# Kernel optimization log

Hardware: AMD Instinct MI355X
Metric: run time of the kernel (lower is better)

## Reference

```python
import jax, jax.numpy as jnp
import numpy as np

B, S, H, M = 8, 128, 768, 128
EPS = 1e-12


def setup_inputs() -> dict:
    key = jax.random.key(0)
    ks = jax.random.split(key, 8)
    seq_hiddens = jax.random.normal(ks[0], (B, S, H), dtype=jnp.float32)
    gamma = jnp.ones((H,), jnp.float32)
    beta = jnp.zeros((H,), jnp.float32)
    # conditional LN dense weights (torch Linear weight: (out, in)); small init so math stays stable
    w_beta = jax.random.normal(ks[1], (H, H), dtype=jnp.float32) * 0.02
    w_gamma = jax.random.normal(ks[2], (H, H), dtype=jnp.float32) * 0.02
    w_ent = jax.random.normal(ks[3], (H, M), dtype=jnp.float32) * 0.02
    w_head = jax.random.normal(ks[4], (H, M), dtype=jnp.float32) * 0.02
    w_tail = jax.random.normal(ks[5], (H, M), dtype=jnp.float32) * 0.02
    b_ent = jnp.zeros((M,), jnp.float32)
    b_head = jnp.zeros((M,), jnp.float32)
    b_tail = jnp.zeros((M,), jnp.float32)
    return dict(seq_hiddens=seq_hiddens, gamma=gamma, beta=beta, w_beta=w_beta,
                w_gamma=w_gamma, w_ent=w_ent, b_ent=b_ent, w_head=w_head,
                b_head=b_head, w_tail=w_tail, b_tail=b_tail)


def _handshake_cln(seq, gamma, beta, w_beta, w_gamma):
    # Triangular pair expansion in the same row-major order as the torch loop:
    # for ind in range(S): pairs (ind, ind), (ind, ind+1), ..., (ind, S-1)
    s = seq.shape[1]
    ii, jj = jnp.triu_indices(s)                 # (P,) each, P = S(S+1)/2
    x = seq[:, jj, :]                            # visible hiddens   (B, P, H)
    cond = seq[:, ii, :]                         # repeated hiddens  (B, P, H)
    beta_c = jnp.einsum('bph,oh->bpo', cond, w_beta) + beta      # (B, P, H)
    gamma_c = jnp.einsum('bph,oh->bpo', cond, w_gamma) + gamma   # (B, P, H)
    mean = jnp.mean(x, axis=-1, keepdims=True)
    out = x - mean
    var = jnp.mean(out * out, axis=-1, keepdims=True)
    std = (var + EPS) ** 2                       # NOTE: faithful to source (no sqrt)
    return out / std * gamma_c + beta_c


def reference(seq_hiddens, gamma, beta, w_beta, w_gamma, w_ent, b_ent,
              w_head, b_head, w_tail, b_tail):
    shaking = _handshake_cln(seq_hiddens, gamma, beta, w_beta, w_gamma)  # (B, P, H)
    ent = jnp.tanh(shaking @ w_ent + b_ent)      # (B, P, M)
    head = jnp.tanh(shaking @ w_head + b_head)
    tail = jnp.tanh(shaking @ w_tail + b_tail)
    return jnp.stack([ent, head, tail], axis=0)  # (3, B, P, M)
```

## Files before the change

### kernel.cpp

```cpp
#include <hip/hip_runtime.h>
#include <hip/hip_bf16.h>
#include <hip/hip_fp16.h>
#include <math.h>

#define B_   8
#define S_   128
#define H_   768
#define M_   128
#define P_   8256
#define BP_  66048
#define EPSF 1e-12f

typedef unsigned short u16;
typedef unsigned int   u32;
typedef _Float16 h16;
typedef _Float16 ffrag __attribute__((ext_vector_type(8)));
typedef float    f32x16 __attribute__((ext_vector_type(16)));

__device__ __forceinline__ u32 fuse2(u32 x, u32 g, u32 b) {
    __half2 r = __hfma2(__builtin_bit_cast(__half2, x),
                        __builtin_bit_cast(__half2, g),
                        __builtin_bit_cast(__half2, b));
    return __builtin_bit_cast(u32, r);
}
__device__ __forceinline__ float fast_tanh(float v) {
    float t = __expf(v + v);
    float r = __builtin_amdgcn_rcpf(t + 1.0f);
    return fmaf(-2.0f, r, 1.0f);
}
__device__ __forceinline__ void gl_lds16(const h16* g, h16* l) {
    __builtin_amdgcn_global_load_lds(
        (const __attribute__((address_space(1))) u32*)g,
        (__attribute__((address_space(3))) u32*)l, 16, 0, 0);
}

#define NORM0 5763
__global__ void k_prep(const float* __restrict__ seq,
                       const float* __restrict__ wg, const float* __restrict__ wb,
                       const float* __restrict__ we, const float* __restrict__ wh,
                       const float* __restrict__ wt,
                       const float* __restrict__ be, const float* __restrict__ bh,
                       const float* __restrict__ bt,
                       h16* __restrict__ wgb, h16* __restrict__ wbb,
                       h16* __restrict__ wpk, float* __restrict__ biasc,
                       h16* __restrict__ xn, h16* __restrict__ condb)
{
    __shared__ float red[4];
    const int bx = blockIdx.x;
    const int t = threadIdx.x;

    if (bx < NORM0) {
        int idx = bx * 256 + t;
        if (idx < 589824) {
            wgb[idx] = (h16)wg[idx];
        } else if (idx < 1179648) {
            int i = idx - 589824;
            wbb[i] = (h16)wb[i];
        } else if (idx < 1474560) {
            int i = idx - 1179648;
            int e  = i & 7;
            int n  = (i >> 3) & 127;
            int v  = i >> 10;
            int ch = v & 3;
            int w2 = v >> 2;
            int kt = w2 % 24;
            int nb = w2 / 24;
            int h  = kt * 32 + ch * 8 + e;
            const float* src = (nb == 0) ? we : (nb == 1 ? wh : wt);
            wpk[i] = (h16)src[h * 128 + n];
        } else if (idx < 1474944) {
            int n = idx - 1474560;
            biasc[n] = (n < 128) ? be[n] : (n < 256 ? bh[n - 128] : bt[n - 256]);
        }
        return;
    }
    const int row = bx - NORM0;
    const int lane = t & 63, wid = t >> 6;
    const float* x = seq + (size_t)row * H_;
    float x0 = x[t], x1 = x[t + 256], x2 = x[t + 512];

    float s = x0 + x1 + x2;
    for (int o = 32; o; o >>= 1) s += __shfl_xor(s, o);
    if (lane == 0) red[wid] = s;
    __syncthreads();
    float mean = (red[0] + red[1] + red[2] + red[3]) * (1.0f / 768.0f);

    float c0 = x0 - mean, c1 = x1 - mean, c2 = x2 - mean;
    float ss = c0 * c0 + c1 * c1 + c2 * c2;
    for (int o = 32; o; o >>= 1) ss += __shfl_xor(ss, o);
    __syncthreads();
    if (lane == 0) red[wid] = ss;
    __syncthreads();
    float var = (red[0] + red[1] + red[2] + red[3]) * (1.0f / 768.0f);
    float sd = var + EPSF;
    float scale = 1.0f / (sd * sd);

    h16* xr = xn + (size_t)row * H_;
    h16* cr = condb + (size_t)row * H_;
    xr[t] = (h16)(c0 * scale); xr[t + 256] = (h16)(c1 * scale); xr[t + 512] = (h16)(c2 * scale);
    cr[t] = (h16)x0;           cr[t + 256] = (h16)x1;           cr[t + 512] = (h16)x2;
}

__global__ __launch_bounds__(256) void k_cond_gemm(
    const h16* __restrict__ Ab, const h16* __restrict__ Wg, const h16* __restrict__ Wb,
    const float* __restrict__ gamma, const float* __restrict__ beta,
    h16* __restrict__ Gc, h16* __restrict__ Bc)
{
    __shared__ h16 Ash[64 * 72];
    __shared__ h16 Bsh[32 * 72];
    const int t = threadIdx.x;
    const int row0 = blockIdx.x * 64;
    const int by = blockIdx.y;
    const bool isg = (by < 24);
    const int nc0 = (isg ? by : by - 24) * 32;
    const h16* wsrc = isg ? Wg : Wb;

    const int r = t >> 2, q = t & 3;
    const h16* ap = Ab + (size_t)(row0 + r) * H_ + q * 16;
    h16* asto = &Ash[r * 72 + q * 16];
    const int rb = t >> 3, qb = t & 7;
    const h16* wp = wsrc + (size_t)(nc0 + rb) * H_ + qb * 8;
    h16* bsto = &Bsh[rb * 72 + qb * 8];

    const int lane = t & 63, wid = t >> 6;
    const int wm0 = (wid >> 1) * 32, wn0 = (wid & 1) * 16;
    const int l15 = lane & 15, quad = lane >> 4, q8 = quad * 8;

    typedef float f32x4 __attribute__((ext_vector_type(4)));
    f32x4 acc[2] = {};
    for (int kt = 0; kt < 12; ++kt) {
        const int k0 = kt * 64;
        uint4 a0 = *(const uint4*)(ap + k0); uint4 a1 = *(const uint4*)(ap + k0 + 8);
        uint4 w0 = *(const uint4*)(wp + k0);
        *(uint4*)asto = a0; *(uint4*)(asto + 8) = a1;
        *(uint4*)bsto = w0;
        __syncthreads();
#pragma unroll
        for (int ks = 0; ks < 64; ks += 32) {
            ffrag af[2], bf;
#pragma unroll
            for (int mi = 0; mi < 2; ++mi)
                af[mi] = *reinterpret_cast<const ffrag*>(&Ash[(wm0 + mi * 16 + l15) * 72 + ks + q8]);
            bf = *reinterpret_cast<const ffrag*>(&Bsh[(wn0 + l15) * 72 + ks + q8]);
#pragma unroll
            for (int mi = 0; mi < 2; ++mi)
                acc[mi] = __builtin_amdgcn_mfma_f32_16x16x32_f16(af[mi], bf, acc[mi], 0, 0, 0);
        }
        __syncthreads();
    }

    const float* bias = isg ? gamma : beta;
    h16* outp = isg ? Gc : Bc;
#pragma unroll
    for (int mi = 0; mi < 2; ++mi) {
        int c = wn0 + l15;
        float bv = bias[nc0 + c];
#pragma unroll
        for (int reg = 0; reg < 4; ++reg) {
            int rg = wm0 + mi * 16 + quad * 4 + reg;
            outp[(size_t)(row0 + rg) * H_ + nc0 + c] = (h16)(acc[mi][reg] + bv);
        }
    }
}

__global__ __launch_bounds__(256, 6) void k_pair_gemm(
    const h16* __restrict__ Xn, const h16* __restrict__ Gcb, const h16* __restrict__ Bcb,
    const h16* __restrict__ Wpk, const float* __restrict__ biasc,
    float* __restrict__ out)
{
    __shared__ h16 Ash[2][4 * 64 * 8];
    __shared__ h16 Bsh[2][4 * 128 * 8];

    const int t = threadIdx.x;
    const int nb = blockIdx.x;
    const int row0 = blockIdx.y * 64;

    const int r_s = t >> 2, c4 = t & 3;
    int gp = row0 + r_s;
    int b = gp / P_;
    int p = gp - b * P_;
    int i = (int)((257.0f - sqrtf(66049.0f - 8.0f * (float)p)) * 0.5f);
    if (i < 0) i = 0; if (i > 127) i = 127;
    while (i > 0 && (i * (257 - i)) / 2 > p) --i;
    while (((i + 1) * (256 - i)) / 2 <= p) ++i;
    int j = i + (p - (i * (257 - i)) / 2);

    const h16* xp  = Xn  + (size_t)(b * 128 + j) * H_ + c4 * 8;
    const h16* gp_ = Gcb + (size_t)(b * 128 + i) * H_ + c4 * 8;
    const h16* bp_ = Bcb + (size_t)(b * 128 + i) * H_ + c4 * 8;
    const int aw = (c4 * 64 + r_s) * 8;

    const h16* wtile = Wpk + (size_t)nb * 24 * 4096;
    const int wud = t & ~63;

    const int lane = t & 63, wid = t >> 6;
    const int wm0 = (wid >> 1) * 32, wn0 = (wid & 1) * 64;
    const int l31 = lane & 31, hi = lane >> 5;

#pragma unroll
    for (int c = 0; c < 2; ++c)
        gl_lds16(wtile + (size_t)(c * 256 + t) * 8, &Bsh[0][(c * 256 + wud) * 8]);
    {
        uint4 xa = *(const uint4*)xp;
        uint4 ga = *(const uint4*)gp_;
        uint4 ba = *(const uint4*)bp_;
        uint4 f;
        f.x = fuse2(xa.x, ga.x, ba.x); f.y = fuse2(xa.y, ga.y, ba.y);
        f.z = fuse2(xa.z, ga.z, ba.z); f.w = fuse2(xa.w, ga.w, ba.w);
        *(uint4*)&Ash[0][aw] = f;
    }
    __syncthreads();

    f32x16 acc[2] = {};
#pragma unroll 2
    for (int kt = 0; kt < 24; ++kt) {
        const int buf = kt & 1, nbf = buf ^ 1;
        uint4 xa, ga, ba;
        if (kt < 23) {
            const h16* wnext = wtile + (size_t)(kt + 1) * 4096;
#pragma unroll
            for (int c = 0; c < 2; ++c)
                gl_lds16(wnext + (size_t)(c * 256 + t) * 8, &Bsh[nbf][(c * 256 + wud) * 8]);
            const int k0 = (kt + 1) * 32;
            xa = *(const uint4*)(xp + k0);
            ga = *(const uint4*)(gp_ + k0);
            ba = *(const uint4*)(bp_ + k0);
        }

#pragma unroll
        for (int ks = 0; ks < 2; ++ks) {
            const int ch0 = ks * 2;
            ffrag af, bf[2];
            af = *reinterpret_cast<const ffrag*>(
                &Ash[buf][((ch0 + hi) * 64 + wm0 + l31) * 8]);
#pragma unroll
            for (int ni = 0; ni < 2; ++ni)
                bf[ni] = *reinterpret_cast<const ffrag*>(
                    &Bsh[buf][((ch0 + hi) * 128 + wn0 + ni * 32 + l31) * 8]);
#pragma unroll
            for (int ni = 0; ni < 2; ++ni)
                acc[ni] = __builtin_amdgcn_mfma_f32_32x32x16_f16(af, bf[ni], acc[ni], 0, 0, 0);
        }

        if (kt < 23) {
            uint4 f;
            f.x = fuse2(xa.x, ga.x, ba.x); f.y = fuse2(xa.y, ga.y, ba.y);
            f.z = fuse2(xa.z, ga.z, ba.z); f.w = fuse2(xa.w, ga.w, ba.w);
            *(uint4*)&Ash[nbf][aw] = f;
        }
        __syncthreads();
    }

#pragma unroll
    for (int ni = 0; ni < 2; ++ni) {
        int c = wn0 + ni * 32 + l31;
        float bv = biasc[nb * 128 + c];
#pragma unroll
        for (int reg = 0; reg < 16; ++reg) {
            int rg = wm0 + (reg & 3) + 8 * (reg >> 2) + 4 * hi;
            out[((size_t)nb * BP_ + row0 + rg) * M_ + c] = fast_tanh(acc[ni][reg] + bv);
        }
    }
}

extern "C" void kernel_launch(void* const* d_in, const int* in_sizes, int n_in,
                              void* d_out, int out_size, void* d_ws, size_t ws_size,
                              hipStream_t stream)
{
    const float* seq     = (const float*)d_in[0];
    const float* gamma   = (const float*)d_in[1];
    const float* beta    = (const float*)d_in[2];
    const float* w_beta  = (const float*)d_in[3];
    const float* w_gamma = (const float*)d_in[4];
    const float* w_ent   = (const float*)d_in[5];
    const float* b_ent   = (const float*)d_in[6];
    const float* w_head  = (const float*)d_in[7];
    const float* b_head  = (const float*)d_in[8];
    const float* w_tail  = (const float*)d_in[9];
    const float* b_tail  = (const float*)d_in[10];
    float* out = (float*)d_out;

    char* ws = (char*)d_ws;
    h16* xn    = (h16*)ws; ws += (size_t)1024 * 768 * 2;
    h16* condb = (h16*)ws; ws += (size_t)1024 * 768 * 2;
    h16* wgb   = (h16*)ws; ws += (size_t)768 * 768 * 2;
    h16* wbb   = (h16*)ws; ws += (size_t)768 * 768 * 2;
    h16* wpk   = (h16*)ws; ws += (size_t)294912 * 2;
    h16* gc    = (h16*)ws; ws += (size_t)1024 * 768 * 2;
    h16* bc    = (h16*)ws; ws += (size_t)1024 * 768 * 2;
    float* biasc = (float*)ws; ws += 384 * 4;

    hipLaunchKernelGGL(k_prep, dim3(NORM0 + 1024), dim3(256), 0, stream,
                       seq, w_gamma, w_beta, w_ent, w_head, w_tail,
                       b_ent, b_head, b_tail, wgb, wbb, wpk, biasc, xn, condb);
    hipLaunchKernelGGL(k_cond_gemm, dim3(16, 48), dim3(256), 0, stream,
                       condb, wgb, wbb, gamma, beta, gc, bc);
    hipLaunchKernelGGL(k_pair_gemm, dim3(3, 1032), dim3(256), 0, stream,
                       xn, gc, bc, wpk, biasc, out);
}
```

Before: 201.5 us.

## Widen pair GEMM tile to all three heads and convert cond weights inline

The pair GEMM now uses 512-thread blocks covering 128 rows by all 384 output columns (ent, head and tail together), with the weight pack reordered to match. Each fused-LN A tile is therefore built once instead of three times, removing redundant gathers and FMA work. Separately, the cond GEMM reads fp32 seq and weights and converts them to fp16 while staging into LDS, dropping the prep-stage fp16 copies of seq and the two square weight matrices. The cost is more LDS and registers per block (six 32x32 accumulators per wave), lower occupancy, and only 516 blocks in the grid.

Result: slower. 219.8 us (+9.1%).

```diff
diff --git a/kernel.cpp b/kernel.cpp
--- a/kernel.cpp
+++ b/kernel.cpp
@@ -33,45 +33,45 @@
         (const __attribute__((address_space(1))) u32*)g,
         (__attribute__((address_space(3))) u32*)l, 16, 0, 0);
 }
-
-#define NORM0 5763
+__device__ __forceinline__ uint4 cvt8(float4 a, float4 b) {
+    h16 v[8];
+    v[0] = (h16)a.x; v[1] = (h16)a.y; v[2] = (h16)a.z; v[3] = (h16)a.w;
+    v[4] = (h16)b.x; v[5] = (h16)b.y; v[6] = (h16)b.z; v[7] = (h16)b.w;
+    return *reinterpret_cast<uint4*>(v);
+}
+
+#define WPKB  1152
+#define NORM0 1154
 __global__ void k_prep(const float* __restrict__ seq,
-                       const float* __restrict__ wg, const float* __restrict__ wb,
                        const float* __restrict__ we, const float* __restrict__ wh,
                        const float* __restrict__ wt,
                        const float* __restrict__ be, const float* __restrict__ bh,
                        const float* __restrict__ bt,
-                       h16* __restrict__ wgb, h16* __restrict__ wbb,
                        h16* __restrict__ wpk, float* __restrict__ biasc,
-                       h16* __restrict__ xn, h16* __restrict__ condb)
+                       h16* __restrict__ xn)
 {
     __shared__ float red[4];
     const int bx = blockIdx.x;
     const int t = threadIdx.x;
 
+    if (bx < WPKB) {
+        int i  = bx * 256 + t;
+        int e  = i & 7;
+        int u  = i >> 3;
+        int n  = u % 384;
+        int w2 = u / 384;
+        int ch = w2 & 3;
+        int kt = w2 >> 2;
+        int h  = kt * 32 + ch * 8 + e;
+        int head = n >> 7, m = n & 127;
+        const float* src = (head == 0) ? we : (head == 1 ? wh : wt);
+        wpk[i] = (h16)src[h * 128 + m];
+        return;
+    }
     if (bx < NORM0) {
-        int idx = bx * 256 + t;
-        if (idx < 589824) {
-            wgb[idx] = (h16)wg[idx];
-        } else if (idx < 1179648) {
-            int i = idx - 589824;
-            wbb[i] = (h16)wb[i];
-        } else if (idx < 1474560) {
-            int i = idx - 1179648;
-            int e  = i & 7;
-            int n  = (i >> 3) & 127;
-            int v  = i >> 10;
-            int ch = v & 3;
-            int w2 = v >> 2;
-            int kt = w2 % 24;
-            int nb = w2 / 24;
-            int h  = kt * 32 + ch * 8 + e;
-            const float* src = (nb == 0) ? we : (nb == 1 ? wh : wt);
-            wpk[i] = (h16)src[h * 128 + n];
-        } else if (idx < 1474944) {
-            int n = idx - 1474560;
+        int n = (bx - WPKB) * 256 + t;
+        if (n < 384)
             biasc[n] = (n < 128) ? be[n] : (n < 256 ? bh[n - 128] : bt[n - 256]);
-        }
         return;
     }
     const int row = bx - NORM0;
@@ -96,13 +96,11 @@
     float scale = 1.0f / (sd * sd);
 
     h16* xr = xn + (size_t)row * H_;
-    h16* cr = condb + (size_t)row * H_;
     xr[t] = (h16)(c0 * scale); xr[t + 256] = (h16)(c1 * scale); xr[t + 512] = (h16)(c2 * scale);
-    cr[t] = (h16)x0;           cr[t + 256] = (h16)x1;           cr[t + 512] = (h16)x2;
 }
 
 __global__ __launch_bounds__(256) void k_cond_gemm(
-    const h16* __restrict__ Ab, const h16* __restrict__ Wg, const h16* __restrict__ Wb,
+    const float* __restrict__ Seq, const float* __restrict__ Wg, const float* __restrict__ Wb,
     const float* __restrict__ gamma, const float* __restrict__ beta,
     h16* __restrict__ Gc, h16* __restrict__ Bc)
 {
@@ -113,13 +111,13 @@
     const int by = blockIdx.y;
     const bool isg = (by < 24);
     const int nc0 = (isg ? by : by - 24) * 32;
-    const h16* wsrc = isg ? Wg : Wb;
+    const float* wsrc = isg ? Wg : Wb;
 
     const int r = t >> 2, q = t & 3;
-    const h16* ap = Ab + (size_t)(row0 + r) * H_ + q * 16;
+    const float* ap = Seq + (size_t)(row0 + r) * H_ + q * 16;
     h16* asto = &Ash[r * 72 + q * 16];
     const int rb = t >> 3, qb = t & 7;
-    const h16* wp = wsrc + (size_t)(nc0 + rb) * H_ + qb * 8;
+    const float* wp = wsrc + (size_t)(nc0 + rb) * H_ + qb * 8;
     h16* bsto = &Bsh[rb * 72 + qb * 8];
 
     const int lane = t & 63, wid = t >> 6;
@@ -130,10 +128,11 @@
     f32x4 acc[2] = {};
     for (int kt = 0; kt < 12; ++kt) {
         const int k0 = kt * 64;
-        uint4 a0 = *(const uint4*)(ap + k0); uint4 a1 = *(const uint4*)(ap + k0 + 8);
-        uint4 w0 = *(const uint4*)(wp + k0);
-        *(uint4*)asto = a0; *(uint4*)(asto + 8) = a1;
-        *(uint4*)bsto = w0;
+        float4 a0 = *(const float4*)(ap + k0);      float4 a1 = *(const float4*)(ap + k0 + 4);
+        float4 a2 = *(const float4*)(ap + k0 + 8);  float4 a3 = *(const float4*)(ap + k0 + 12);
+        float4 w0 = *(const float4*)(wp + k0);      float4 w1 = *(const float4*)(wp + k0 + 4);
+        *(uint4*)asto = cvt8(a0, a1); *(uint4*)(asto + 8) = cvt8(a2, a3);
+        *(uint4*)bsto = cvt8(w0, w1);
         __syncthreads();
 #pragma unroll
         for (int ks = 0; ks < 64; ks += 32) {
@@ -163,19 +162,18 @@
     }
 }
 
-__global__ __launch_bounds__(256, 6) void k_pair_gemm(
+__global__ __launch_bounds__(512, 2) void k_pair_gemm(
     const h16* __restrict__ Xn, const h16* __restrict__ Gcb, const h16* __restrict__ Bcb,
     const h16* __restrict__ Wpk, const float* __restrict__ biasc,
     float* __restrict__ out)
 {
-    __shared__ h16 Ash[2][4 * 64 * 8];
-    __shared__ h16 Bsh[2][4 * 128 * 8];
+    __shared__ h16 Ash[2][4 * 128 * 8];
+    __shared__ h16 Bsh[2][4 * 384 * 8];
 
     const int t = threadIdx.x;
-    const int nb = blockIdx.x;
-    const int row0 = blockIdx.y * 64;
-
-    const int r_s = t >> 2, c4 = t & 3;
+    const int row0 = blockIdx.x * 128;
+
+    const int r_s = t >> 2, q = t & 3;
     int gp = row0 + r_s;
     int b = gp / P_;
     int p = gp - b * P_;
@@ -185,21 +183,20 @@
     while (((i + 1) * (256 - i)) / 2 <= p) ++i;
     int j = i + (p - (i * (257 - i)) / 2);
 
-    const h16* xp  = Xn  + (size_t)(b * 128 + j) * H_ + c4 * 8;
-    const h16* gp_ = Gcb + (size_t)(b * 128 + i) * H_ + c4 * 8;
-    const h16* bp_ = Bcb + (size_t)(b * 128 + i) * H_ + c4 * 8;
-    const int aw = (c4 * 64 + r_s) * 8;
-
-    const h16* wtile = Wpk + (size_t)nb * 24 * 4096;
+    const h16* xp  = Xn  + (size_t)(b * 128 + j) * H_ + q * 8;
+    const h16* gp_ = Gcb + (size_t)(b * 128 + i) * H_ + q * 8;
+    const h16* bp_ = Bcb + (size_t)(b * 128 + i) * H_ + q * 8;
+    const int aw = (q * 128 + r_s) * 8;
+
     const int wud = t & ~63;
 
     const int lane = t & 63, wid = t >> 6;
-    const int wm0 = (wid >> 1) * 32, wn0 = (wid & 1) * 64;
+    const int wm0 = (wid >> 2) * 64, wn0 = (wid & 3) * 96;
     const int l31 = lane & 31, hi = lane >> 5;
 
 #pragma unroll
-    for (int c = 0; c < 2; ++c)
-        gl_lds16(wtile + (size_t)(c * 256 + t) * 8, &Bsh[0][(c * 256 + wud) * 8]);
+    for (int c = 0; c < 3; ++c)
+        gl_lds16(Wpk + (size_t)(c * 512 + t) * 8, &Bsh[0][(c * 512 + wud) * 8]);
     {
         uint4 xa = *(const uint4*)xp;
         uint4 ga = *(const uint4*)gp_;
@@ -211,16 +208,16 @@
     }
     __syncthreads();
 
-    f32x16 acc[2] = {};
+    f32x16 acc[2][3] = {};
 #pragma unroll 2
     for (int kt = 0; kt < 24; ++kt) {
         const int buf = kt & 1, nbf = buf ^ 1;
         uint4 xa, ga, ba;
         if (kt < 23) {
-            const h16* wnext = wtile + (size_t)(kt + 1) * 4096;
-#pragma unroll
-            for (int c = 0; c < 2; ++c)
-                gl_lds16(wnext + (size_t)(c * 256 + t) * 8, &Bsh[nbf][(c * 256 + wud) * 8]);
+            const h16* wnext = Wpk + (size_t)(kt + 1) * 12288;
+#pragma unroll
+            for (int c = 0; c < 3; ++c)
+                gl_lds16(wnext + (size_t)(c * 512 + t) * 8, &Bsh[nbf][(c * 512 + wud) * 8]);
             const int k0 = (kt + 1) * 32;
             xa = *(const uint4*)(xp + k0);
             ga = *(const uint4*)(gp_ + k0);
@@ -230,16 +227,20 @@
 #pragma unroll
         for (int ks = 0; ks < 2; ++ks) {
             const int ch0 = ks * 2;
-            ffrag af, bf[2];
-            af = *reinterpret_cast<const ffrag*>(
-                &Ash[buf][((ch0 + hi) * 64 + wm0 + l31) * 8]);
-#pragma unroll
-            for (int ni = 0; ni < 2; ++ni)
+            ffrag af[2], bf[3];
+#pragma unroll
+            for (int mi = 0; mi < 2; ++mi)
+                af[mi] = *reinterpret_cast<const ffrag*>(
+                    &Ash[buf][((ch0 + hi) * 128 + wm0 + mi * 32 + l31) * 8]);
+#pragma unroll
+            for (int ni = 0; ni < 3; ++ni)
                 bf[ni] = *reinterpret_cast<const ffrag*>(
-                    &Bsh[buf][((ch0 + hi) * 128 + wn0 + ni * 32 + l31) * 8]);
-#pragma unroll
-            for (int ni = 0; ni < 2; ++ni)
-                acc[ni] = __builtin_amdgcn_mfma_f32_32x32x16_f16(af, bf[ni], acc[ni], 0, 0, 0);
+                    &Bsh[buf][((ch0 + hi) * 384 + wn0 + ni * 32 + l31) * 8]);
+#pragma unroll
+            for (int mi = 0; mi < 2; ++mi)
+#pragma unroll
+                for (int ni = 0; ni < 3; ++ni)
+                    acc[mi][ni] = __builtin_amdgcn_mfma_f32_32x32x16_f16(af[mi], bf[ni], acc[mi][ni], 0, 0, 0);
         }
 
         if (kt < 23) {
@@ -252,15 +253,18 @@
     }
 
 #pragma unroll
-    for (int ni = 0; ni < 2; ++ni) {
-        int c = wn0 + ni * 32 + l31;
-        float bv = biasc[nb * 128 + c];
-#pragma unroll
-        for (int reg = 0; reg < 16; ++reg) {
-            int rg = wm0 + (reg & 3) + 8 * (reg >> 2) + 4 * hi;
-            out[((size_t)nb * BP_ + row0 + rg) * M_ + c] = fast_tanh(acc[ni][reg] + bv);
-        }
-    }
+    for (int mi = 0; mi < 2; ++mi)
+#pragma unroll
+        for (int ni = 0; ni < 3; ++ni) {
+            int c = wn0 + ni * 32 + l31;
+            int head = c >> 7, m = c & 127;
+            float bv = biasc[c];
+#pragma unroll
+            for (int reg = 0; reg < 16; ++reg) {
+                int rg = wm0 + mi * 32 + (reg & 3) + 8 * (reg >> 2) + 4 * hi;
+                out[((size_t)head * BP_ + row0 + rg) * M_ + m] = fast_tanh(acc[mi][ni][reg] + bv);
+            }
+        }
 }
 
 extern "C" void kernel_launch(void* const* d_in, const int* in_sizes, int n_in,
@@ -282,19 +286,16 @@
 
     char* ws = (char*)d_ws;
     h16* xn    = (h16*)ws; ws += (size_t)1024 * 768 * 2;
-    h16* condb = (h16*)ws; ws += (size_t)1024 * 768 * 2;
-    h16* wgb   = (h16*)ws; ws += (size_t)768 * 768 * 2;
-    h16* wbb   = (h16*)ws; ws += (size_t)768 * 768 * 2;
     h16* wpk   = (h16*)ws; ws += (size_t)294912 * 2;
     h16* gc    = (h16*)ws; ws += (size_t)1024 * 768 * 2;
     h16* bc    = (h16*)ws; ws += (size_t)1024 * 768 * 2;
     float* biasc = (float*)ws; ws += 384 * 4;
 
     hipLaunchKernelGGL(k_prep, dim3(NORM0 + 1024), dim3(256), 0, stream,
-                       seq, w_gamma, w_beta, w_ent, w_head, w_tail,
-                       b_ent, b_head, b_tail, wgb, wbb, wpk, biasc, xn, condb);
+                       seq, w_ent, w_head, w_tail,
+                       b_ent, b_head, b_tail, wpk, biasc, xn);
     hipLaunchKernelGGL(k_cond_gemm, dim3(16, 48), dim3(256), 0, stream,
-                       condb, wgb, wbb, gamma, beta, gc, bc);
-    hipLaunchKernelGGL(k_pair_gemm, dim3(3, 1032), dim3(256), 0, stream,
+                       seq, w_gamma, w_beta, gamma, beta, gc, bc);
+    hipLaunchKernelGGL(k_pair_gemm, dim3(516), dim3(512), 0, stream,
                        xn, gc, bc, wpk, biasc, out);
 }
```

## Fuse conditional GEMM into prep kernel with on-the-fly fp32-to-fp16 conversion

Applied to the files above, without the earlier changes.

The conditional-LN GEMM now runs inside the prep kernel. It reads fp32 seq and weights straight from global memory and converts them to fp16 while writing LDS, so the intermediate fp16 copies of the weights and cond rows are no longer materialised. The output-weight packing is redone with an LDS-staged transpose so that global reads and writes are vectorised. This removes one kernel launch and several HBM round-trips. In exchange the GEMM loads twice as many bytes per tile, and the enlarged 48KB shared-memory allocation may lower occupancy for the normalisation blocks.

Measured after the change: 203.1 us. No clear change (+0.8%).

```diff
diff --git a/kernel.cpp b/kernel.cpp
--- a/kernel.cpp
+++ b/kernel.cpp
@@ -33,47 +33,126 @@
         (const __attribute__((address_space(1))) u32*)g,
         (__attribute__((address_space(3))) u32*)l, 16, 0, 0);
 }
-
-#define NORM0 5763
-__global__ void k_prep(const float* __restrict__ seq,
-                       const float* __restrict__ wg, const float* __restrict__ wb,
-                       const float* __restrict__ we, const float* __restrict__ wh,
-                       const float* __restrict__ wt,
-                       const float* __restrict__ be, const float* __restrict__ bh,
-                       const float* __restrict__ bt,
-                       h16* __restrict__ wgb, h16* __restrict__ wbb,
-                       h16* __restrict__ wpk, float* __restrict__ biasc,
-                       h16* __restrict__ xn, h16* __restrict__ condb)
+__device__ __forceinline__ uint4 cvt8(float4 a, float4 b) {
+    h16 v[8];
+    v[0] = (h16)a.x; v[1] = (h16)a.y; v[2] = (h16)a.z; v[3] = (h16)a.w;
+    v[4] = (h16)b.x; v[5] = (h16)b.y; v[6] = (h16)b.z; v[7] = (h16)b.w;
+    return *reinterpret_cast<uint4*>(v);
+}
+
+#define CONDB 768
+#define WPK0  768
+#define BIAS0 792
+#define NORM0 794
+__global__ __launch_bounds__(256) void k_pre(
+    const float* __restrict__ seq,
+    const float* __restrict__ wg, const float* __restrict__ wb,
+    const float* __restrict__ we, const float* __restrict__ wh,
+    const float* __restrict__ wt,
+    const float* __restrict__ gamma, const float* __restrict__ beta,
+    const float* __restrict__ be, const float* __restrict__ bh,
+    const float* __restrict__ bt,
+    h16* __restrict__ wpk, float* __restrict__ biasc,
+    h16* __restrict__ xn, h16* __restrict__ Gc, h16* __restrict__ Bc)
 {
-    __shared__ float red[4];
+    __shared__ __align__(16) char smem[49152];
     const int bx = blockIdx.x;
     const int t = threadIdx.x;
 
+    if (bx < CONDB) {
+        h16* Ash = (h16*)smem;
+        h16* Bsh = (h16*)smem + 64 * 72;
+        const int rbx = bx & 15, by = bx >> 4;
+        const int row0 = rbx * 64;
+        const bool isg = (by < 24);
+        const int nc0 = (isg ? by : by - 24) * 32;
+        const float* wsrc = isg ? wg : wb;
+
+        const int r = t >> 2, q = t & 3;
+        const float* ap = seq + (size_t)(row0 + r) * H_ + q * 16;
+        h16* asto = &Ash[r * 72 + q * 16];
+        const int rb = t >> 3, qb = t & 7;
+        const float* wp = wsrc + (size_t)(nc0 + rb) * H_ + qb * 8;
+        h16* bsto = &Bsh[rb * 72 + qb * 8];
+
+        const int lane = t & 63, wid = t >> 6;
+        const int wm0 = (wid >> 1) * 32, wn0 = (wid & 1) * 16;
+        const int l15 = lane & 15, quad = lane >> 4, q8 = quad * 8;
+
+        typedef float f32x4 __attribute__((ext_vector_type(4)));
+        f32x4 acc[2] = {};
+        for (int kt = 0; kt < 12; ++kt) {
+            const int k0 = kt * 64;
+            float4 a0 = *(const float4*)(ap + k0);      float4 a1 = *(const float4*)(ap + k0 + 4);
+            float4 a2 = *(const float4*)(ap + k0 + 8);  float4 a3 = *(const float4*)(ap + k0 + 12);
+            float4 w0 = *(const float4*)(wp + k0);      float4 w1 = *(const float4*)(wp + k0 + 4);
+            *(uint4*)asto = cvt8(a0, a1); *(uint4*)(asto + 8) = cvt8(a2, a3);
+            *(uint4*)bsto = cvt8(w0, w1);
+            __syncthreads();
+#pragma unroll
+            for (int ks = 0; ks < 64; ks += 32) {
+                ffrag af[2], bf;
+#pragma unroll
+                for (int mi = 0; mi < 2; ++mi)
+                    af[mi] = *reinterpret_cast<const ffrag*>(&Ash[(wm0 + mi * 16 + l15) * 72 + ks + q8]);
+                bf = *reinterpret_cast<const ffrag*>(&Bsh[(wn0 + l15) * 72 + ks + q8]);
+#pragma unroll
+                for (int mi = 0; mi < 2; ++mi)
+                    acc[mi] = __builtin_amdgcn_mfma_f32_16x16x32_f16(af[mi], bf, acc[mi], 0, 0, 0);
+            }
+            __syncthreads();
+        }
+
+        const float* bias = isg ? gamma : beta;
+        h16* outp = isg ? Gc : Bc;
+#pragma unroll
+        for (int mi = 0; mi < 2; ++mi) {
+            int c = wn0 + l15;
+            float bv = bias[nc0 + c];
+#pragma unroll
+            for (int reg = 0; reg < 4; ++reg) {
+                int rg = wm0 + mi * 16 + quad * 4 + reg;
+                outp[(size_t)(row0 + rg) * H_ + nc0 + c] = (h16)(acc[mi][reg] + bv);
+            }
+        }
+        return;
+    }
+
+    if (bx < BIAS0) {
+        const int kt = bx - WPK0;
+        float* stage = (float*)smem;
+        int f = t;
+#pragma unroll
+        for (int k = 0; k < 12; ++k, f += 256) {
+            int head = f >> 10, rem = f & 1023;
+            int h = rem >> 5, m4 = rem & 31;
+            const float* src = (head == 0) ? we : (head == 1 ? wh : wt);
+            *(float4*)(stage + (size_t)f * 4) =
+                *(const float4*)(src + (size_t)(kt * 32 + h) * 128 + m4 * 4);
+        }
+        __syncthreads();
+#pragma unroll
+        for (int rr = 0; rr < 6; ++rr) {
+            int s = t + 256 * rr;
+            int nb = s >> 9, rem = s & 511;
+            int ch = rem >> 7, nl = rem & 127;
+            h16 v[8];
+#pragma unroll
+            for (int e = 0; e < 8; ++e)
+                v[e] = (h16)stage[(size_t)((nb * 32 + ch * 8 + e) * 128 + nl)];
+            *(uint4*)(wpk + (size_t)nb * 98304 + kt * 4096 + (ch * 128 + nl) * 8) = *(uint4*)v;
+        }
+        return;
+    }
+
     if (bx < NORM0) {
-        int idx = bx * 256 + t;
-        if (idx < 589824) {
-            wgb[idx] = (h16)wg[idx];
-        } else if (idx < 1179648) {
-            int i = idx - 589824;
-            wbb[i] = (h16)wb[i];
-        } else if (idx < 1474560) {
-            int i = idx - 1179648;
-            int e  = i & 7;
-            int n  = (i >> 3) & 127;
-            int v  = i >> 10;
-            int ch = v & 3;
-            int w2 = v >> 2;
-            int kt = w2 % 24;
-            int nb = w2 / 24;
-            int h  = kt * 32 + ch * 8 + e;
-            const float* src = (nb == 0) ? we : (nb == 1 ? wh : wt);
-            wpk[i] = (h16)src[h * 128 + n];
-        } else if (idx < 1474944) {
-            int n = idx - 1474560;
+        int n = (bx - BIAS0) * 256 + t;
+        if (n < 384)
             biasc[n] = (n < 128) ? be[n] : (n < 256 ? bh[n - 128] : bt[n - 256]);
-        }
         return;
     }
+
+    float* red = (float*)smem;
     const int row = bx - NORM0;
     const int lane = t & 63, wid = t >> 6;
     const float* x = seq + (size_t)row * H_;
@@ -96,71 +175,7 @@
     float scale = 1.0f / (sd * sd);
 
     h16* xr = xn + (size_t)row * H_;
-    h16* cr = condb + (size_t)row * H_;
     xr[t] = (h16)(c0 * scale); xr[t + 256] = (h16)(c1 * scale); xr[t + 512] = (h16)(c2 * scale);
-    cr[t] = (h16)x0;           cr[t + 256] = (h16)x1;           cr[t + 512] = (h16)x2;
-}
-
-__global__ __launch_bounds__(256) void k_cond_gemm(
-    const h16* __restrict__ Ab, const h16* __restrict__ Wg, const h16* __restrict__ Wb,
-    const float* __restrict__ gamma, const float* __restrict__ beta,
-    h16* __restrict__ Gc, h16* __restrict__ Bc)
-{
-    __shared__ h16 Ash[64 * 72];
-    __shared__ h16 Bsh[32 * 72];
-    const int t = threadIdx.x;
-    const int row0 = blockIdx.x * 64;
-    const int by = blockIdx.y;
-    const bool isg = (by < 24);
-    const int nc0 = (isg ? by : by - 24) * 32;
-    const h16* wsrc = isg ? Wg : Wb;
-
-    const int r = t >> 2, q = t & 3;
-    const h16* ap = Ab + (size_t)(row0 + r) * H_ + q * 16;
-    h16* asto = &Ash[r * 72 + q * 16];
-    const int rb = t >> 3, qb = t & 7;
-    const h16* wp = wsrc + (size_t)(nc0 + rb) * H_ + qb * 8;
-    h16* bsto = &Bsh[rb * 72 + qb * 8];
-
-    const int lane = t & 63, wid = t >> 6;
-    const int wm0 = (wid >> 1) * 32, wn0 = (wid & 1) * 16;
-    const int l15 = lane & 15, quad = lane >> 4, q8 = quad * 8;
-
-    typedef float f32x4 __attribute__((ext_vector_type(4)));
-    f32x4 acc[2] = {};
-    for (int kt = 0; kt < 12; ++kt) {
-        const int k0 = kt * 64;
-        uint4 a0 = *(const uint4*)(ap + k0); uint4 a1 = *(const uint4*)(ap + k0 + 8);
-        uint4 w0 = *(const uint4*)(wp + k0);
-        *(uint4*)asto = a0; *(uint4*)(asto + 8) = a1;
-        *(uint4*)bsto = w0;
-        __syncthreads();
-#pragma unroll
-        for (int ks = 0; ks < 64; ks += 32) {
-            ffrag af[2], bf;
-#pragma unroll
-            for (int mi = 0; mi < 2; ++mi)
-                af[mi] = *reinterpret_cast<const ffrag*>(&Ash[(wm0 + mi * 16 + l15) * 72 + ks + q8]);
-            bf = *reinterpret_cast<const ffrag*>(&Bsh[(wn0 + l15) * 72 + ks + q8]);
-#pragma unroll
-            for (int mi = 0; mi < 2; ++mi)
-                acc[mi] = __builtin_amdgcn_mfma_f32_16x16x32_f16(af[mi], bf, acc[mi], 0, 0, 0);
-        }
-        __syncthreads();
-    }
-
-    const float* bias = isg ? gamma : beta;
-    h16* outp = isg ? Gc : Bc;
-#pragma unroll
-    for (int mi = 0; mi < 2; ++mi) {
-        int c = wn0 + l15;
-        float bv = bias[nc0 + c];
-#pragma unroll
-        for (int reg = 0; reg < 4; ++reg) {
-            int rg = wm0 + mi * 16 + quad * 4 + reg;
-            outp[(size_t)(row0 + rg) * H_ + nc0 + c] = (h16)(acc[mi][reg] + bv);
-        }
-    }
 }
 
 __global__ __launch_bounds__(256, 6) void k_pair_gemm(
@@ -282,19 +297,15 @@
 
     char* ws = (char*)d_ws;
     h16* xn    = (h16*)ws; ws += (size_t)1024 * 768 * 2;
-    h16* condb = (h16*)ws; ws += (size_t)1024 * 768 * 2;
-    h16* wgb   = (h16*)ws; ws += (size_t)768 * 768 * 2;
-    h16* wbb   = (h16*)ws; ws += (size_t)768 * 768 * 2;
     h16* wpk   = (h16*)ws; ws += (size_t)294912 * 2;
     h16* gc    = (h16*)ws; ws += (size_t)1024 * 768 * 2;
     h16* bc    = (h16*)ws; ws += (size_t)1024 * 768 * 2;
     float* biasc = (float*)ws; ws += 384 * 4;
 
-    hipLaunchKernelGGL(k_prep, dim3(NORM0 + 1024), dim3(256), 0, stream,
+    hipLaunchKernelGGL(k_pre, dim3(NORM0 + 1024), dim3(256), 0, stream,
                        seq, w_gamma, w_beta, w_ent, w_head, w_tail,
-                       b_ent, b_head, b_tail, wgb, wbb, wpk, biasc, xn, condb);
-    hipLaunchKernelGGL(k_cond_gemm, dim3(16, 48), dim3(256), 0, stream,
-                       condb, wgb, wbb, gamma, beta, gc, bc);
+                       gamma, beta, b_ent, b_head, b_tail,
+                       wpk, biasc, xn, gc, bc);
     hipLaunchKernelGGL(k_pair_gemm, dim3(3, 1032), dim3(256), 0, stream,
                        xn, gc, bc, wpk, biasc, out);
 }
```
